# Kernel tuning notes

Measured on AMD Instinct MI355X. Metric: run time of the kernel, lower is better.

## Reference

```python
import jax, jax.numpy as jnp
import numpy as np

E = 512        # embedding_dim
DM = 512       # d_model
H = 8          # num_heads
HD = DM // H   # head_dim
NL = 4         # (e_num_layers-1) + (d_num_layers-1) identical VaeEncoder blocks
CIN = 32       # input_dim
EPS = 1e-5


def setup_inputs() -> dict:
    key = jax.random.key(0)
    ks = jax.random.split(key, 8)
    s = 0.02
    n = lambda k, shape: jax.random.normal(k, shape, jnp.float32) * s
    return {
        "x": jax.random.normal(ks[0], (4, 2048, CIN), jnp.float32),
        "conv_w": n(ks[1], (E, CIN, 3)),
        "conv_b": jnp.zeros((E,), jnp.float32),
        "qkv_w": n(ks[2], (NL, 3 * DM, E)),
        "qkv_b": jnp.zeros((NL, 3 * DM), jnp.float32),
        "out_w": n(ks[3], (NL, E, DM)),
        "out_b": jnp.zeros((NL, E), jnp.float32),
        "fc1_w": n(ks[4], (NL, E, E)),
        "fc1_b": jnp.zeros((NL, E), jnp.float32),
        "fc2_w": n(ks[5], (NL, E, E)),
        "fc2_b": jnp.zeros((NL, E), jnp.float32),
        "ln1_w": jnp.ones((NL, E), jnp.float32),
        "ln1_b": jnp.zeros((NL, E), jnp.float32),
        "ln2_w": jnp.ones((NL, E), jnp.float32),
        "ln2_b": jnp.zeros((NL, E), jnp.float32),
        "outp_w": n(ks[6], (CIN, E)),
        "outp_b": jnp.zeros((CIN,), jnp.float32),
    }


def _pos_embedding(L, d):
    pos = jnp.arange(L, dtype=jnp.float32)[:, None]
    div = jnp.exp(jnp.arange(0, d, 2, dtype=jnp.float32) * (-np.log(10000.0) / d))
    pe = jnp.zeros((L, d), jnp.float32)
    pe = pe.at[:, 0::2].set(jnp.sin(pos * div))
    pe = pe.at[:, 1::2].set(jnp.cos(pos * div))
    return pe


def _layernorm(x, w, b):
    mu = jnp.mean(x, axis=-1, keepdims=True)
    xc = x - mu
    inv = jax.lax.rsqrt(jnp.mean(xc * xc, axis=-1, keepdims=True) + EPS)
    return xc * inv * w + b


def _encoder_block(x, p):
    (qkv_w, qkv_b, out_w, out_b, fc1_w, fc1_b, fc2_w, fc2_b,
     ln1_w, ln1_b, ln2_w, ln2_b) = p
    B, L, _ = x.shape
    qkv = x @ qkv_w.T + qkv_b                      # [B, L, 3*DM]
    q = qkv[:, :, :DM].reshape(B, L, H, HD)
    k = qkv[:, :, DM:2 * DM].reshape(B, L, H, HD)
    v = qkv[:, :, 2 * DM:].reshape(B, L, H, HD)
    scores = jnp.einsum('bqhd,bkhd->bhqk', q, k)   # [B, H, L, L]
    attn = jax.nn.softmax(scores / jnp.sqrt(jnp.float32(HD)), axis=-1)
    ctx = jnp.einsum('bhqk,bkhd->bqhd', attn, v).reshape(B, L, DM)
    x = _layernorm(x + (ctx @ out_w.T + out_b), ln1_w, ln1_b)
    h = jax.nn.silu(x @ fc1_w.T + fc1_b) @ fc2_w.T + fc2_b
    return _layernorm(x + h, ln2_w, ln2_b)


def reference(x, conv_w, conv_b, qkv_w, qkv_b, out_w, out_b,
              fc1_w, fc1_b, fc2_w, fc2_b, ln1_w, ln1_b, ln2_w, ln2_b,
              outp_w, outp_b):
    B, L, _ = x.shape
    # TokenEmbedding: circular Conv1d k=3 pad=1 over the time axis
    xc = jnp.pad(x.transpose(0, 2, 1), ((0, 0), (0, 0), (1, 1)), mode='wrap')
    h = jax.lax.conv_general_dilated(
        xc, conv_w, (1,), 'VALID',
        dimension_numbers=('NCH', 'OIH', 'NCH')) + conv_b[None, :, None]
    h = h.transpose(0, 2, 1) + _pos_embedding(L, E)[None]
    params = (qkv_w, qkv_b, out_w, out_b, fc1_w, fc1_b, fc2_w, fc2_b,
              ln1_w, ln1_b, ln2_w, ln2_b)
    def step(carry, p):
        return _encoder_block(carry, p), None
    h, _ = jax.lax.scan(step, h, params)
    return h @ outp_w.T + outp_b
```

## Files before the change

kernel.cpp:

```cpp
#include <hip/hip_runtime.h>
#include <hip/hip_bf16.h>
#include <cstddef>

typedef short bf16x8 __attribute__((ext_vector_type(8)));
typedef float f32x4 __attribute__((ext_vector_type(4)));

__device__ __forceinline__ unsigned short f2bf(float x) {
  __hip_bfloat16 h = __float2bfloat16(x);
  unsigned short u; __builtin_memcpy(&u, &h, 2); return u;
}
__device__ __forceinline__ float bf2f(unsigned short u) {
  unsigned int v = ((unsigned int)u) << 16; float f; __builtin_memcpy(&f, &v, 4); return f;
}
__device__ __forceinline__ float swz16f(float x) {
  int i; __builtin_memcpy(&i, &x, 4);
  i = __builtin_amdgcn_ds_swizzle(i, 0x401F);
  float r; __builtin_memcpy(&r, &i, 4); return r;
}
__device__ __forceinline__ void gload16(const unsigned short* g, unsigned short* l) {
  __builtin_amdgcn_global_load_lds(
      (const __attribute__((address_space(1))) void*)g,
      (__attribute__((address_space(3))) void*)l, 16, 0, 0);
}
__device__ __forceinline__ void pipe_sync() {
  asm volatile("s_waitcnt vmcnt(0)" ::: "memory");
  __builtin_amdgcn_s_barrier();
  __builtin_amdgcn_sched_barrier(0);
}
__device__ __forceinline__ void bar_only() {
  asm volatile("" ::: "memory");
  __builtin_amdgcn_s_barrier();
  __builtin_amdgcn_sched_barrier(0);
}

__global__ __launch_bounds__(256) void cvt_all(
    const float* __restrict__ qkv_w, const float* __restrict__ out_w,
    const float* __restrict__ fc1_w, const float* __restrict__ fc2_w,
    const float* __restrict__ outp_w, unsigned short* __restrict__ dst)
{
  int i = blockIdx.x * 256 + threadIdx.x;
  if (i >= 1576960) return;
  const float* src; int off;
  if (i < 786432)       { src = qkv_w;  off = i; }
  else if (i < 1048576) { src = out_w;  off = i - 786432; }
  else if (i < 1310720) { src = fc1_w;  off = i - 1048576; }
  else if (i < 1572864) { src = fc2_w;  off = i - 1310720; }
  else                  { src = outp_w; off = i - 1572864; }
  float4 v = *(const float4*)(src + (size_t)off * 4);
  ushort4 o;
  o.x = f2bf(v.x); o.y = f2bf(v.y); o.z = f2bf(v.z); o.w = f2bf(v.w);
  *(ushort4*)(dst + (size_t)i * 4) = o;
}

__global__ __launch_bounds__(256) void conv_pe_kernel(
    const float* __restrict__ x, const float* __restrict__ cw,
    const float* __restrict__ cb, unsigned short* __restrict__ outb)
{
  const int L = 2048, CIN = 32;
  int b  = blockIdx.x >> 8;
  int l0 = (blockIdx.x & 255) << 3;
  int t  = threadIdx.x;
  __shared__ float xs[10][32];
  for (int idx = t; idx < 320; idx += 256) {
    int rr = idx >> 5, ci = idx & 31;
    int gl = (l0 - 1 + rr + L) & (L - 1);
    xs[rr][ci] = x[((size_t)b * L + gl) * CIN + ci];
  }
  __syncthreads();
  int e0 = t << 1;
  float acc0[8], acc1[8];
  float bb0 = cb[e0], bb1 = cb[e0 + 1];
#pragma unroll
  for (int li = 0; li < 8; li++) { acc0[li] = bb0; acc1[li] = bb1; }
  const float* w0p = cw + (size_t)e0 * 96;
  const float* w1p = w0p + 96;
  for (int ci = 0; ci < 32; ci++) {
#pragma unroll
    for (int kk = 0; kk < 3; kk++) {
      float w0 = w0p[ci * 3 + kk];
      float w1 = w1p[ci * 3 + kk];
#pragma unroll
      for (int li = 0; li < 8; li++) {
        float xv = xs[li + kk][ci];
        acc0[li] += xv * w0;
        acc1[li] += xv * w1;
      }
    }
  }
  float dv = __expf((float)e0 * (-9.210340371976184f / 512.0f));
#pragma unroll
  for (int li = 0; li < 8; li++) {
    int l = l0 + li;
    float arg = (float)l * dv;
    float sv = sinf(arg), cv = cosf(arg);
    size_t off = ((size_t)b * L + l) * 512 + e0;
    ushort2 ob; ob.x = f2bf(acc0[li] + sv); ob.y = f2bf(acc1[li] + cv);
    *(ushort2*)&outb[off] = ob;
  }
}

template<int EPI, int QSCALE, int NFR, int VOUT>
__global__ __launch_bounds__(256) void gemm_bf(
    const unsigned short* __restrict__ X,
    const unsigned short* __restrict__ W,
    const float* __restrict__ bias,
    const unsigned short* __restrict__ R,
    unsigned short* __restrict__ Yb,
    float* __restrict__ Yf,
    unsigned short* __restrict__ VT,
    int N)
{
  const int K = 512;
  constexpr int BN = NFR * 32;
  constexpr int WB = NFR * 4096;
  constexpr int BUF = 16384 + WB;
  __shared__ __align__(16) char smem[2 * BUF];
  int t = threadIdx.x;
  int lane = t & 63, wv = t >> 6;
  int g = lane >> 4, li = lane & 15;
  int m0 = (blockIdx.x & 63) << 7;
  int n0 = (blockIdx.x >> 6) * BN;
  int wm = (wv >> 1) << 6;
  int wn = (wv & 1) * (BN / 2);

  int subrow = lane >> 3;
  int coloff = ((lane & 7) ^ subrow) << 3;

  f32x4 acc[4][NFR];
#pragma unroll
  for (int a = 0; a < 4; a++)
#pragma unroll
    for (int b2 = 0; b2 < NFR; b2++) acc[a][b2] = (f32x4){0.f, 0.f, 0.f, 0.f};

#pragma unroll
  for (int j = 0; j < 4; j++) {
    int row = (wv * 4 + j) * 8 + subrow;
    gload16(X + (size_t)(m0 + row) * K + coloff,
            (unsigned short*)(smem + (wv * 4 + j) * 1024));
  }
#pragma unroll
  for (int j = 0; j < NFR; j++) {
    int row = (wv * NFR + j) * 8 + subrow;
    gload16(W + (size_t)(n0 + row) * K + coloff,
            (unsigned short*)(smem + 16384 + (wv * NFR + j) * 1024));
  }

#pragma unroll
  for (int ks = 0; ks < 8; ks++) {
    const int buf = ks & 1;
    char* cur = smem + buf * BUF;
    if (ks < 7) {
      char* nxt = smem + (buf ^ 1) * BUF;
      int k0 = (ks + 1) * 64;
#pragma unroll
      for (int j = 0; j < 4; j++) {
        int row = (wv * 4 + j) * 8 + subrow;
        gload16(X + (size_t)(m0 + row) * K + k0 + coloff,
                (unsigned short*)(nxt + (wv * 4 + j) * 1024));
      }
#pragma unroll
      for (int j = 0; j < NFR; j++) {
        int row = (wv * NFR + j) * 8 + subrow;
        gload16(W + (size_t)(n0 + row) * K + k0 + coloff,
                (unsigned short*)(nxt + 16384 + (wv * NFR + j) * 1024));
      }
      if constexpr (NFR == 4) asm volatile("s_waitcnt vmcnt(8)" ::: "memory");
      else if constexpr (NFR == 2) asm volatile("s_waitcnt vmcnt(6)" ::: "memory");
      else asm volatile("s_waitcnt vmcnt(5)" ::: "memory");
    } else {
      asm volatile("s_waitcnt vmcnt(0)" ::: "memory");
    }
    __builtin_amdgcn_s_barrier();
    __builtin_amdgcn_sched_barrier(0);

#pragma unroll
    for (int s = 0; s < 2; s++) {
      bf16x8 af[4], bfr[NFR];
#pragma unroll
      for (int mt = 0; mt < 4; mt++) {
        int row = wm + 16 * mt + li;
        af[mt] = *(const bf16x8*)(cur + (row * 8 + ((g + 4 * s) ^ (row & 7))) * 16);
      }
#pragma unroll
      for (int nt = 0; nt < NFR; nt++) {
        int row = wn + 16 * nt + li;
        bfr[nt] = *(const bf16x8*)(cur + 16384 +
                                   (row * 8 + ((g + 4 * s) ^ (row & 7))) * 16);
      }
#pragma unroll
      for (int mt = 0; mt < 4; mt++)
#pragma unroll
        for (int nt = 0; nt < NFR; nt++)
          acc[mt][nt] = __builtin_amdgcn_mfma_f32_16x16x32_bf16(
              af[mt], bfr[nt], acc[mt][nt], 0, 0, 0);
    }
    if (ks < 7) bar_only();
  }

  float bv[NFR];
#pragma unroll
  for (int nt = 0; nt < NFR; nt++) bv[nt] = bias[n0 + wn + 16 * nt + li];

  if (VOUT && n0 >= 1024) {
    unsigned short* Ts = (unsigned short*)smem;
    __builtin_amdgcn_s_barrier();
#pragma unroll
    for (int nt = 0; nt < NFR; nt++) {
      int col = wn + 16 * nt + li;
      float bvn = bv[nt];
#pragma unroll
      for (int mt = 0; mt < 4; mt++) {
        float v0 = acc[mt][nt][0] + bvn, v1 = acc[mt][nt][1] + bvn;
        float v2 = acc[mt][nt][2] + bvn, v3 = acc[mt][nt][3] + bvn;
        uint2 pk;
        asm("v_cvt_pk_bf16_f32 %0, %1, %2" : "=v"(pk.x) : "v"(v0), "v"(v1));
        asm("v_cvt_pk_bf16_f32 %0, %1, %2" : "=v"(pk.y) : "v"(v2), "v"(v3));
        *(uint2*)(Ts + col * 136 + wm + 16 * mt + 4 * g) = pk;
      }
    }
    __syncthreads();
    int vcol = t >> 1, half = t & 1;
    int gc = n0 - 1024 + vcol;
    int bh = (m0 >> 11) * 8 + (gc >> 6);
    int d  = gc & 63;
    unsigned short* dst = VT + ((size_t)bh * 64 + d) * 2048 + (m0 & 2047) + half * 64;
    const unsigned short* srcp = Ts + vcol * 136 + half * 64;
#pragma unroll
    for (int j2 = 0; j2 < 8; j2++)
      *(bf16x8*)(dst + j2 * 8) = *(const bf16x8*)(srcp + j2 * 8);
    return;
  }

#pragma unroll
  for (int mt = 0; mt < 4; mt++) {
#pragma unroll
    for (int i = 0; i < 4; i++) {
      size_t roff = (size_t)(m0 + wm + 16 * mt + 4 * g + i) * N;
#pragma unroll
      for (int nt = 0; nt < NFR; nt++) {
        int col = n0 + wn + 16 * nt + li;
        float v = acc[mt][nt][i] + bv[nt];
        if (EPI == 1) {
          v += bf2f(R[roff + col]);
          Yb[roff + col] = f2bf(v);
        } else if (EPI == 2) {
          v = v / (1.f + __expf(-v));
          Yb[roff + col] = f2bf(v);
        } else if (EPI == 3) {
          Yf[roff + col] = v;
        } else {
          if (QSCALE && col < 512) v *= 0.18033688011112042f;
          Yb[roff + col] = f2bf(v);
        }
      }
    }
  }
}

__global__ __launch_bounds__(256) void attn_mfma(
    const unsigned short* __restrict__ qkv,
    const unsigned short* __restrict__ Vt,
    unsigned short* __restrict__ ctx)
{
  const int L = 2048;
  int bh = blockIdx.x & 31, qi = blockIdx.x >> 5;
  int b = bh >> 3, h = bh & 7;
  int q0 = qi << 7;
  size_t tb = (size_t)b * L;
  int t = threadIdx.x, lane = t & 63, wv = t >> 6;
  int g = lane >> 4, li = lane & 15;
  int lisw = li & 7;

  __shared__ __align__(16) char smem[81920];

  int wq = q0 + wv * 32;
  bf16x8 qf00, qf01, qf10, qf11;
  {
    const unsigned short* qp0 = qkv + (tb + wq + li) * 1536 + h * 64 + g * 8;
    qf00 = *(const bf16x8*)qp0;
    qf01 = *(const bf16x8*)(qp0 + 32);
    const unsigned short* qp1 = qp0 + (size_t)16 * 1536;
    qf10 = *(const bf16x8*)qp1;
    qf11 = *(const bf16x8*)(qp1 + 32);
  }

  f32x4 accA[4], accB[4];
#pragma unroll
  for (int nt = 0; nt < 4; nt++) {
    accA[nt] = (f32x4){0.f, 0.f, 0.f, 0.f};
    accB[nt] = (f32x4){0.f, 0.f, 0.f, 0.f};
  }
  float lA = 0.f, lB = 0.f;

  int koff0 = li * 128 + ((g    ) ^ lisw) * 16;
  int koff1 = li * 128 + ((g + 4) ^ lisw) * 16;
  int vrowb = 16384 + li * 256;
  int vs00 = ((g    ) ^ lisw) << 4;
  int vs01 = ((g + 4) ^ lisw) << 4;
  int vs10 = ((8 + g) ^ lisw) << 4;
  int vs11 = ((12 + g) ^ lisw) << 4;
  const char* pb0 = smem + 65536 + wv * 4096 + li * 128 + ((g    ) ^ lisw) * 16;
  const char* pb1 = smem + 65536 + wv * 4096 + li * 128 + ((g + 4) ^ lisw) * 16;
  char* pwbase = smem + 65536 + wv * 4096 + li * 128 + ((g & 1) << 3);
  char* pw0 = pwbase + (((0 + (g >> 1)) ^ lisw) << 4);
  char* pw1 = pwbase + (((2 + (g >> 1)) ^ lisw) << 4);
  char* pw2 = pwbase + (((4 + (g >> 1)) ^ lisw) << 4);
  char* pw3 = pwbase + (((6 + (g >> 1)) ^ lisw) << 4);

  int subrow = lane >> 3;
  int coloff = ((lane & 7) ^ subrow) << 3;
  const unsigned short* kp[4];
  const unsigned short* vp[4];
#pragma unroll
  for (int j = 0; j < 4; j++) {
    int krow = (wv * 4 + j) * 8 + subrow;
    kp[j] = qkv + (tb + krow) * 1536 + 512 + h * 64 + coloff;
    int vrow = (wv * 4 + j) * 4 + g;
    vp[j] = Vt + ((size_t)bh * 64 + vrow) * 2048 + ((li ^ (vrow & 7)) << 3);
  }

#pragma unroll
  for (int j = 0; j < 4; j++) {
    gload16(kp[j], (unsigned short*)(smem + (wv * 4 + j) * 1024));
    gload16(vp[j], (unsigned short*)(smem + 16384 + (wv * 4 + j) * 1024));
    kp[j] += (size_t)128 * 1536; vp[j] += 128;
  }
  pipe_sync();

#pragma unroll 2
  for (int it = 0; it < 16; it++) {
    const int buf = it & 1;
    const char* base = smem + buf * 32768;
    if (it < 15) {
      char* nb = smem + (buf ^ 1) * 32768;
#pragma unroll
      for (int j = 0; j < 4; j++) {
        gload16(kp[j], (unsigned short*)(nb + (wv * 4 + j) * 1024));
        gload16(vp[j], (unsigned short*)(nb + 16384 + (wv * 4 + j) * 1024));
        kp[j] += (size_t)128 * 1536; vp[j] += 128;
      }
    }

    f32x4 sA[8], sB[8];
#pragma unroll
    for (int mt = 0; mt < 8; mt++) {
      sA[mt] = (f32x4){0.f, 0.f, 0.f, 0.f};
      sB[mt] = (f32x4){0.f, 0.f, 0.f, 0.f};
    }
    __builtin_amdgcn_s_setprio(1);
#pragma unroll
    for (int mt = 0; mt < 8; mt++) {
      bf16x8 kf = *(const bf16x8*)(base + koff0 + mt * 2048);
      sA[mt] = __builtin_amdgcn_mfma_f32_16x16x32_bf16(kf, qf00, sA[mt], 0, 0, 0);
      sB[mt] = __builtin_amdgcn_mfma_f32_16x16x32_bf16(kf, qf10, sB[mt], 0, 0, 0);
    }
#pragma unroll
    for (int mt = 0; mt < 8; mt++) {
      bf16x8 kf = *(const bf16x8*)(base + koff1 + mt * 2048);
      sA[mt] = __builtin_amdgcn_mfma_f32_16x16x32_bf16(kf, qf01, sA[mt], 0, 0, 0);
      sB[mt] = __builtin_amdgcn_mfma_f32_16x16x32_bf16(kf, qf11, sB[mt], 0, 0, 0);
    }
    __builtin_amdgcn_s_setprio(0);

    float psA = 0.f, psB = 0.f;
#define PBLK(SARR, PS, PWP, OFF)                                              \
    {                                                                         \
      float p0 = SARR[0], p1 = SARR[1], p2 = SARR[2], p3 = SARR[3];           \
      asm volatile("v_exp_f32 %0, %0\n\tv_exp_f32 %1, %1\n\t"                 \
                   "v_exp_f32 %2, %2\n\tv_exp_f32 %3, %3\n\ts_nop 1"          \
                   : "+v"(p0), "+v"(p1), "+v"(p2), "+v"(p3));                 \
      PS += (p0 + p1) + (p2 + p3);                                            \
      uint2 pv;                                                               \
      asm("v_cvt_pk_bf16_f32 %0, %1, %2" : "=v"(pv.x) : "v"(p0), "v"(p1));    \
      asm("v_cvt_pk_bf16_f32 %0, %1, %2" : "=v"(pv.y) : "v"(p2), "v"(p3));    \
      *(uint2*)(PWP + OFF) = pv;                                              \
    }
    PBLK(sA[0], psA, pw0, 0) PBLK(sA[1], psA, pw1, 0)
    PBLK(sA[2], psA, pw2, 0) PBLK(sA[3], psA, pw3, 0)
    PBLK(sB[0], psB, pw0, 2048) PBLK(sB[1], psB, pw1, 2048)
    PBLK(sB[2], psB, pw2, 2048) PBLK(sB[3], psB, pw3, 2048)
    {
      bf16x8 paA0 = *(const bf16x8*)(pb0);
      bf16x8 paB0 = *(const bf16x8*)(pb0 + 2048);
      __builtin_amdgcn_s_setprio(1);
#pragma unroll
      for (int nt = 0; nt < 4; nt++) {
        bf16x8 vb = *(const bf16x8*)(base + vrowb + nt * 4096 + vs00);
        accA[nt] = __builtin_amdgcn_mfma_f32_16x16x32_bf16(paA0, vb, accA[nt], 0, 0, 0);
        accB[nt] = __builtin_amdgcn_mfma_f32_16x16x32_bf16(paB0, vb, accB[nt], 0, 0, 0);
      }
      __builtin_amdgcn_s_setprio(0);
      bf16x8 paA1 = *(const bf16x8*)(pb1);
      bf16x8 paB1 = *(const bf16x8*)(pb1 + 2048);
      __builtin_amdgcn_s_setprio(1);
#pragma unroll
      for (int nt = 0; nt < 4; nt++) {
        bf16x8 vb = *(const bf16x8*)(base + vrowb + nt * 4096 + vs01);
        accA[nt] = __builtin_amdgcn_mfma_f32_16x16x32_bf16(paA1, vb, accA[nt], 0, 0, 0);
        accB[nt] = __builtin_amdgcn_mfma_f32_16x16x32_bf16(paB1, vb, accB[nt], 0, 0, 0);
      }
      __builtin_amdgcn_s_setprio(0);
    }
    PBLK(sA[4], psA, pw0, 0) PBLK(sA[5], psA, pw1, 0)
    PBLK(sA[6], psA, pw2, 0) PBLK(sA[7], psA, pw3, 0)
    PBLK(sB[4], psB, pw0, 2048) PBLK(sB[5], psB, pw1, 2048)
    PBLK(sB[6], psB, pw2, 2048) PBLK(sB[7], psB, pw3, 2048)
#undef PBLK
    {
      bf16x8 paA0 = *(const bf16x8*)(pb0);
      bf16x8 paB0 = *(const bf16x8*)(pb0 + 2048);
      __builtin_amdgcn_s_setprio(1);
#pragma unroll
      for (int nt = 0; nt < 4; nt++) {
        bf16x8 vb = *(const bf16x8*)(base + vrowb + nt * 4096 + vs10);
        accA[nt] = __builtin_amdgcn_mfma_f32_16x16x32_bf16(paA0, vb, accA[nt], 0, 0, 0);
        accB[nt] = __builtin_amdgcn_mfma_f32_16x16x32_bf16(paB0, vb, accB[nt], 0, 0, 0);
      }
      __builtin_amdgcn_s_setprio(0);
      bf16x8 paA1 = *(const bf16x8*)(pb1);
      bf16x8 paB1 = *(const bf16x8*)(pb1 + 2048);
      __builtin_amdgcn_s_setprio(1);
#pragma unroll
      for (int nt = 0; nt < 4; nt++) {
        bf16x8 vb = *(const bf16x8*)(base + vrowb + nt * 4096 + vs11);
        accA[nt] = __builtin_amdgcn_mfma_f32_16x16x32_bf16(paA1, vb, accA[nt], 0, 0, 0);
        accB[nt] = __builtin_amdgcn_mfma_f32_16x16x32_bf16(paB1, vb, accB[nt], 0, 0, 0);
      }
      __builtin_amdgcn_s_setprio(0);
    }
    psA += swz16f(psA); psA += __shfl_xor(psA, 32); lA += psA;
    psB += swz16f(psB); psB += __shfl_xor(psB, 32); lB += psB;

    pipe_sync();
  }

  float liA[4], liB[4];
#pragma unroll
  for (int i = 0; i < 4; i++) {
    liA[i] = 1.f / __shfl(lA, 4 * g + i);
    liB[i] = 1.f / __shfl(lB, 4 * g + i);
  }
#pragma unroll
  for (int i = 0; i < 4; i++) {
    size_t ra = (tb + wq + 4 * g + i) * 512 + h * 64;
    size_t rb = (tb + wq + 16 + 4 * g + i) * 512 + h * 64;
#pragma unroll
    for (int nt = 0; nt < 4; nt++) {
      ctx[ra + 16 * nt + li] = f2bf(accA[nt][i] * liA[i]);
      ctx[rb + 16 * nt + li] = f2bf(accB[nt][i] * liB[i]);
    }
  }
}

__global__ __launch_bounds__(256) void ln_kernel(
    const unsigned short* __restrict__ X, const float* __restrict__ g,
    const float* __restrict__ b, unsigned short* __restrict__ Yb)
{
  int t = threadIdx.x, lane = t & 63, wv = t >> 6;
  size_t row = (size_t)blockIdx.x * 4 + wv;
  bf16x8 xv = *(const bf16x8*)(X + row * 512 + lane * 8);
  float xf[8];
#pragma unroll
  for (int j = 0; j < 8; j++) xf[j] = bf2f((unsigned short)xv[j]);
  float sum = 0.f, sq = 0.f;
#pragma unroll
  for (int j = 0; j < 8; j++) { sum += xf[j]; sq += xf[j] * xf[j]; }
#pragma unroll
  for (int off = 32; off > 0; off >>= 1) {
    sum += __shfl_xor(sum, off);
    sq  += __shfl_xor(sq, off);
  }
  float mu  = sum * (1.0f / 512.0f);
  float inv = rsqrtf(sq * (1.0f / 512.0f) - mu * mu + 1e-5f);
  float4 g0 = *(const float4*)(g + lane * 8);
  float4 g1 = *(const float4*)(g + lane * 8 + 4);
  float4 b0 = *(const float4*)(b + lane * 8);
  float4 b1 = *(const float4*)(b + lane * 8 + 4);
  float gw[8] = {g0.x, g0.y, g0.z, g0.w, g1.x, g1.y, g1.z, g1.w};
  float bw[8] = {b0.x, b0.y, b0.z, b0.w, b1.x, b1.y, b1.z, b1.w};
  bf16x8 yb;
#pragma unroll
  for (int j = 0; j < 8; j++)
    yb[j] = (short)f2bf((xf[j] - mu) * inv * gw[j] + bw[j]);
  *(bf16x8*)(Yb + row * 512 + lane * 8) = yb;
}

extern "C" void kernel_launch(void* const* d_in, const int* in_sizes, int n_in,
                              void* d_out, int out_size, void* d_ws, size_t ws_size,
                              hipStream_t stream) {
  (void)in_sizes; (void)n_in; (void)out_size; (void)ws_size;
  const float* x      = (const float*)d_in[0];
  const float* conv_w = (const float*)d_in[1];
  const float* conv_b = (const float*)d_in[2];
  const float* qkv_w  = (const float*)d_in[3];
  const float* qkv_b  = (const float*)d_in[4];
  const float* out_w  = (const float*)d_in[5];
  const float* out_b  = (const float*)d_in[6];
  const float* fc1_w  = (const float*)d_in[7];
  const float* fc1_b  = (const float*)d_in[8];
  const float* fc2_w  = (const float*)d_in[9];
  const float* fc2_b  = (const float*)d_in[10];
  const float* ln1_w  = (const float*)d_in[11];
  const float* ln1_b  = (const float*)d_in[12];
  const float* ln2_w  = (const float*)d_in[13];
  const float* ln2_b  = (const float*)d_in[14];
  const float* outp_w = (const float*)d_in[15];
  const float* outp_b = (const float*)d_in[16];
  float* out = (float*)d_out;

  char* p = (char*)d_ws;
  unsigned short* A    = (unsigned short*)p;            p += (size_t)8192 * 512 * 2;
  unsigned short* QKV  = (unsigned short*)p;            p += (size_t)8192 * 1536 * 2;
  unsigned short* VT   = (unsigned short*)p;            p += (size_t)32 * 64 * 2048 * 2;
  unsigned short* CTX  = (unsigned short*)p;            p += (size_t)8192 * 512 * 2;
  unsigned short* Wq   = (unsigned short*)p;            p += (size_t)4 * 1536 * 512 * 2;
  unsigned short* Wo   = (unsigned short*)p;            p += (size_t)4 * 512 * 512 * 2;
  unsigned short* W1   = (unsigned short*)p;            p += (size_t)4 * 512 * 512 * 2;
  unsigned short* W2   = (unsigned short*)p;            p += (size_t)4 * 512 * 512 * 2;
  unsigned short* Wp   = (unsigned short*)p;            p += (size_t)32 * 512 * 2;
  unsigned short* D = QKV;

  cvt_all<<<6160, 256, 0, stream>>>(qkv_w, out_w, fc1_w, fc2_w, outp_w, Wq);

  conv_pe_kernel<<<1024, 256, 0, stream>>>(x, conv_w, conv_b, A);

  for (int l = 0; l < 4; l++) {
    gemm_bf<0, 1, 4, 1><<<64 * 12, 256, 0, stream>>>(
        A, Wq + (size_t)l * 1536 * 512, qkv_b + l * 1536, nullptr,
        QKV, nullptr, VT, 1536);
    attn_mfma<<<512, 256, 0, stream>>>(QKV, VT, CTX);
    gemm_bf<1, 0, 2, 0><<<64 * 8, 256, 0, stream>>>(
        CTX, Wo + (size_t)l * 512 * 512, out_b + l * 512, A,
        D, nullptr, nullptr, 512);
    ln_kernel<<<2048, 256, 0, stream>>>(D, ln1_w + l * 512, ln1_b + l * 512, A);
    gemm_bf<2, 0, 2, 0><<<64 * 8, 256, 0, stream>>>(
        A, W1 + (size_t)l * 512 * 512, fc1_b + l * 512, nullptr,
        CTX, nullptr, nullptr, 512);
    gemm_bf<1, 0, 2, 0><<<64 * 8, 256, 0, stream>>>(
        CTX, W2 + (size_t)l * 512 * 512, fc2_b + l * 512, A,
        D, nullptr, nullptr, 512);
    ln_kernel<<<2048, 256, 0, stream>>>(D, ln2_w + l * 512, ln2_b + l * 512, A);
  }
  gemm_bf<3, 0, 1, 0><<<64, 256, 0, stream>>>(
      A, Wp, outp_b, nullptr, nullptr, out, nullptr, 32);
}
```

Before: 481.4 us.

## Keep softmax probabilities in registers by permuting K rows to match MFMA layout

The attention kernel no longer writes exp'd scores to an LDS scratch region and reads them back as the PV MFMA A-operand. Instead, key rows are assigned to even/odd MFMA tiles with a matching swizzle so each lane's QK accumulator outputs can be packed directly into bf16x8 operands for the PV MFMAs. This removes the LDS round trip for P and shrinks shared memory from 80KB to 64KB, which may allow more resident blocks. The cost is more live registers for sixteen score accumulators and eight packed operands, plus a more intricate K load swizzle that must stay consistent with the V row order.

```diff
diff --git a/kernel.cpp b/kernel.cpp
--- a/kernel.cpp
+++ b/kernel.cpp
@@ -269,9 +269,9 @@
   size_t tb = (size_t)b * L;
   int t = threadIdx.x, lane = t & 63, wv = t >> 6;
   int g = lane >> 4, li = lane & 15;
-  int lisw = li & 7;
-
-  __shared__ __align__(16) char smem[81920];
+  int lisw7 = li & 7;
+
+  __shared__ __align__(16) char smem[65536];
 
   int wq = q0 + wv * 32;
   bf16x8 qf00, qf01, qf10, qf11;
@@ -292,29 +292,27 @@
   }
   float lA = 0.f, lB = 0.f;
 
-  int koff0 = li * 128 + ((g    ) ^ lisw) * 16;
-  int koff1 = li * 128 + ((g + 4) ^ lisw) * 16;
+  int rowE = ((li >> 2) << 3) + (li & 3);
+  int swzE = (li >> 2) << 1;
+  int swzO = swzE + 1;
+  int kE0 = rowE * 128 + ((g ^ swzE) << 4);
+  int kE1 = rowE * 128 + (((g + 4) ^ swzE) << 4);
+  int kO0 = (rowE + 4) * 128 + ((g ^ swzO) << 4);
+  int kO1 = (rowE + 4) * 128 + (((g + 4) ^ swzO) << 4);
   int vrowb = 16384 + li * 256;
-  int vs00 = ((g    ) ^ lisw) << 4;
-  int vs01 = ((g + 4) ^ lisw) << 4;
-  int vs10 = ((8 + g) ^ lisw) << 4;
-  int vs11 = ((12 + g) ^ lisw) << 4;
-  const char* pb0 = smem + 65536 + wv * 4096 + li * 128 + ((g    ) ^ lisw) * 16;
-  const char* pb1 = smem + 65536 + wv * 4096 + li * 128 + ((g + 4) ^ lisw) * 16;
-  char* pwbase = smem + 65536 + wv * 4096 + li * 128 + ((g & 1) << 3);
-  char* pw0 = pwbase + (((0 + (g >> 1)) ^ lisw) << 4);
-  char* pw1 = pwbase + (((2 + (g >> 1)) ^ lisw) << 4);
-  char* pw2 = pwbase + (((4 + (g >> 1)) ^ lisw) << 4);
-  char* pw3 = pwbase + (((6 + (g >> 1)) ^ lisw) << 4);
+  int vsl0 = ((g     ) ^ lisw7) << 4;
+  int vsl1 = ((g +  4) ^ lisw7) << 4;
+  int vsl2 = ((g +  8) ^ lisw7) << 4;
+  int vsl3 = ((g + 12) ^ lisw7) << 4;
 
   int subrow = lane >> 3;
-  int coloff = ((lane & 7) ^ subrow) << 3;
   const unsigned short* kp[4];
   const unsigned short* vp[4];
 #pragma unroll
   for (int j = 0; j < 4; j++) {
     int krow = (wv * 4 + j) * 8 + subrow;
-    kp[j] = qkv + (tb + krow) * 1536 + 512 + h * 64 + coloff;
+    int swzk = (2 * j + (subrow >> 2)) & 7;
+    kp[j] = qkv + (tb + krow) * 1536 + 512 + h * 64 + (((lane & 7) ^ swzk) << 3);
     int vrow = (wv * 4 + j) * 4 + g;
     vp[j] = Vt + ((size_t)bh * 64 + vrow) * 2048 + ((li ^ (vrow & 7)) << 3);
   }
@@ -341,93 +339,76 @@
       }
     }
 
-    f32x4 sA[8], sB[8];
-#pragma unroll
-    for (int mt = 0; mt < 8; mt++) {
-      sA[mt] = (f32x4){0.f, 0.f, 0.f, 0.f};
-      sB[mt] = (f32x4){0.f, 0.f, 0.f, 0.f};
-    }
+    f32x4 sEA0, sEA1, sEA2, sEA3, sOA0, sOA1, sOA2, sOA3;
+    f32x4 sEB0, sEB1, sEB2, sEB3, sOB0, sOB1, sOB2, sOB3;
+    const f32x4 kZ = {0.f, 0.f, 0.f, 0.f};
     __builtin_amdgcn_s_setprio(1);
-#pragma unroll
-    for (int mt = 0; mt < 8; mt++) {
-      bf16x8 kf = *(const bf16x8*)(base + koff0 + mt * 2048);
-      sA[mt] = __builtin_amdgcn_mfma_f32_16x16x32_bf16(kf, qf00, sA[mt], 0, 0, 0);
-      sB[mt] = __builtin_amdgcn_mfma_f32_16x16x32_bf16(kf, qf10, sB[mt], 0, 0, 0);
-    }
-#pragma unroll
-    for (int mt = 0; mt < 8; mt++) {
-      bf16x8 kf = *(const bf16x8*)(base + koff1 + mt * 2048);
-      sA[mt] = __builtin_amdgcn_mfma_f32_16x16x32_bf16(kf, qf01, sA[mt], 0, 0, 0);
-      sB[mt] = __builtin_amdgcn_mfma_f32_16x16x32_bf16(kf, qf11, sB[mt], 0, 0, 0);
-    }
+#define QKC(C, SEA, SOA, SEB, SOB)                                            \
+    {                                                                         \
+      bf16x8 k0 = *(const bf16x8*)(base + (C) * 4096 + kE0);                  \
+      bf16x8 k1 = *(const bf16x8*)(base + (C) * 4096 + kE1);                  \
+      SEA = __builtin_amdgcn_mfma_f32_16x16x32_bf16(k0, qf00, kZ, 0, 0, 0);   \
+      SEB = __builtin_amdgcn_mfma_f32_16x16x32_bf16(k0, qf10, kZ, 0, 0, 0);   \
+      SEA = __builtin_amdgcn_mfma_f32_16x16x32_bf16(k1, qf01, SEA, 0, 0, 0);  \
+      SEB = __builtin_amdgcn_mfma_f32_16x16x32_bf16(k1, qf11, SEB, 0, 0, 0);  \
+      bf16x8 k2 = *(const bf16x8*)(base + (C) * 4096 + kO0);                  \
+      bf16x8 k3 = *(const bf16x8*)(base + (C) * 4096 + kO1);                  \
+      SOA = __builtin_amdgcn_mfma_f32_16x16x32_bf16(k2, qf00, kZ, 0, 0, 0);   \
+      SOB = __builtin_amdgcn_mfma_f32_16x16x32_bf16(k2, qf10, kZ, 0, 0, 0);   \
+      SOA = __builtin_amdgcn_mfma_f32_16x16x32_bf16(k3, qf01, SOA, 0, 0, 0);  \
+      SOB = __builtin_amdgcn_mfma_f32_16x16x32_bf16(k3, qf11, SOB, 0, 0, 0);  \
+    }
+    QKC(0, sEA0, sOA0, sEB0, sOB0)
+    QKC(1, sEA1, sOA1, sEB1, sOB1)
+    QKC(2, sEA2, sOA2, sEB2, sOB2)
+    QKC(3, sEA3, sOA3, sEB3, sOB3)
+#undef QKC
     __builtin_amdgcn_s_setprio(0);
 
     float psA = 0.f, psB = 0.f;
-#define PBLK(SARR, PS, PWP, OFF)                                              \
+    bf16x8 paA0, paA1, paA2, paA3, paB0, paB1, paB2, paB3;
+#define EPACK(SE, SO, PS, PA)                                                 \
     {                                                                         \
-      float p0 = SARR[0], p1 = SARR[1], p2 = SARR[2], p3 = SARR[3];           \
+      float e0 = SE[0], e1 = SE[1], e2 = SE[2], e3 = SE[3];                   \
+      float o0 = SO[0], o1 = SO[1], o2 = SO[2], o3 = SO[3];                   \
       asm volatile("v_exp_f32 %0, %0\n\tv_exp_f32 %1, %1\n\t"                 \
                    "v_exp_f32 %2, %2\n\tv_exp_f32 %3, %3\n\ts_nop 1"          \
-                   : "+v"(p0), "+v"(p1), "+v"(p2), "+v"(p3));                 \
-      PS += (p0 + p1) + (p2 + p3);                                            \
-      uint2 pv;                                                               \
-      asm("v_cvt_pk_bf16_f32 %0, %1, %2" : "=v"(pv.x) : "v"(p0), "v"(p1));    \
-      asm("v_cvt_pk_bf16_f32 %0, %1, %2" : "=v"(pv.y) : "v"(p2), "v"(p3));    \
-      *(uint2*)(PWP + OFF) = pv;                                              \
-    }
-    PBLK(sA[0], psA, pw0, 0) PBLK(sA[1], psA, pw1, 0)
-    PBLK(sA[2], psA, pw2, 0) PBLK(sA[3], psA, pw3, 0)
-    PBLK(sB[0], psB, pw0, 2048) PBLK(sB[1], psB, pw1, 2048)
-    PBLK(sB[2], psB, pw2, 2048) PBLK(sB[3], psB, pw3, 2048)
-    {
-      bf16x8 paA0 = *(const bf16x8*)(pb0);
-      bf16x8 paB0 = *(const bf16x8*)(pb0 + 2048);
-      __builtin_amdgcn_s_setprio(1);
-#pragma unroll
-      for (int nt = 0; nt < 4; nt++) {
-        bf16x8 vb = *(const bf16x8*)(base + vrowb + nt * 4096 + vs00);
-        accA[nt] = __builtin_amdgcn_mfma_f32_16x16x32_bf16(paA0, vb, accA[nt], 0, 0, 0);
-        accB[nt] = __builtin_amdgcn_mfma_f32_16x16x32_bf16(paB0, vb, accB[nt], 0, 0, 0);
-      }
-      __builtin_amdgcn_s_setprio(0);
-      bf16x8 paA1 = *(const bf16x8*)(pb1);
-      bf16x8 paB1 = *(const bf16x8*)(pb1 + 2048);
-      __builtin_amdgcn_s_setprio(1);
-#pragma unroll
-      for (int nt = 0; nt < 4; nt++) {
-        bf16x8 vb = *(const bf16x8*)(base + vrowb + nt * 4096 + vs01);
-        accA[nt] = __builtin_amdgcn_mfma_f32_16x16x32_bf16(paA1, vb, accA[nt], 0, 0, 0);
-        accB[nt] = __builtin_amdgcn_mfma_f32_16x16x32_bf16(paB1, vb, accB[nt], 0, 0, 0);
-      }
-      __builtin_amdgcn_s_setprio(0);
-    }
-    PBLK(sA[4], psA, pw0, 0) PBLK(sA[5], psA, pw1, 0)
-    PBLK(sA[6], psA, pw2, 0) PBLK(sA[7], psA, pw3, 0)
-    PBLK(sB[4], psB, pw0, 2048) PBLK(sB[5], psB, pw1, 2048)
-    PBLK(sB[6], psB, pw2, 2048) PBLK(sB[7], psB, pw3, 2048)
-#undef PBLK
-    {
-      bf16x8 paA0 = *(const bf16x8*)(pb0);
-      bf16x8 paB0 = *(const bf16x8*)(pb0 + 2048);
-      __builtin_amdgcn_s_setprio(1);
-#pragma unroll
-      for (int nt = 0; nt < 4; nt++) {
-        bf16x8 vb = *(const bf16x8*)(base + vrowb + nt * 4096 + vs10);
-        accA[nt] = __builtin_amdgcn_mfma_f32_16x16x32_bf16(paA0, vb, accA[nt], 0, 0, 0);
-        accB[nt] = __builtin_amdgcn_mfma_f32_16x16x32_bf16(paB0, vb, accB[nt], 0, 0, 0);
-      }
-      __builtin_amdgcn_s_setprio(0);
-      bf16x8 paA1 = *(const bf16x8*)(pb1);
-      bf16x8 paB1 = *(const bf16x8*)(pb1 + 2048);
-      __builtin_amdgcn_s_setprio(1);
-#pragma unroll
-      for (int nt = 0; nt < 4; nt++) {
-        bf16x8 vb = *(const bf16x8*)(base + vrowb + nt * 4096 + vs11);
-        accA[nt] = __builtin_amdgcn_mfma_f32_16x16x32_bf16(paA1, vb, accA[nt], 0, 0, 0);
-        accB[nt] = __builtin_amdgcn_mfma_f32_16x16x32_bf16(paB1, vb, accB[nt], 0, 0, 0);
-      }
-      __builtin_amdgcn_s_setprio(0);
-    }
+                   : "+v"(e0), "+v"(e1), "+v"(e2), "+v"(e3));                 \
+      asm volatile("v_exp_f32 %0, %0\n\tv_exp_f32 %1, %1\n\t"                 \
+                   "v_exp_f32 %2, %2\n\tv_exp_f32 %3, %3\n\ts_nop 1"          \
+                   : "+v"(o0), "+v"(o1), "+v"(o2), "+v"(o3));                 \
+      PS += ((e0 + e1) + (e2 + e3)) + ((o0 + o1) + (o2 + o3));                \
+      unsigned int d0, d1, d2, d3;                                            \
+      asm("v_cvt_pk_bf16_f32 %0, %1, %2" : "=v"(d0) : "v"(e0), "v"(e1));      \
+      asm("v_cvt_pk_bf16_f32 %0, %1, %2" : "=v"(d1) : "v"(e2), "v"(e3));      \
+      asm("v_cvt_pk_bf16_f32 %0, %1, %2" : "=v"(d2) : "v"(o0), "v"(o1));      \
+      asm("v_cvt_pk_bf16_f32 %0, %1, %2" : "=v"(d3) : "v"(o2), "v"(o3));      \
+      unsigned int tmp_[4] = {d0, d1, d2, d3};                                \
+      __builtin_memcpy(&PA, tmp_, 16);                                        \
+    }
+    EPACK(sEA0, sOA0, psA, paA0) EPACK(sEA1, sOA1, psA, paA1)
+    EPACK(sEA2, sOA2, psA, paA2) EPACK(sEA3, sOA3, psA, paA3)
+    EPACK(sEB0, sOB0, psB, paB0) EPACK(sEB1, sOB1, psB, paB1)
+    EPACK(sEB2, sOB2, psB, paB2) EPACK(sEB3, sOB3, psB, paB3)
+#undef EPACK
+
+    __builtin_amdgcn_s_setprio(1);
+#define PVC(PAA, PAB, VS)                                                     \
+    {                                                                         \
+      _Pragma("unroll")                                                       \
+      for (int nt = 0; nt < 4; nt++) {                                        \
+        bf16x8 vb = *(const bf16x8*)(base + vrowb + nt * 4096 + (VS));        \
+        accA[nt] = __builtin_amdgcn_mfma_f32_16x16x32_bf16(PAA, vb, accA[nt], 0, 0, 0); \
+        accB[nt] = __builtin_amdgcn_mfma_f32_16x16x32_bf16(PAB, vb, accB[nt], 0, 0, 0); \
+      }                                                                       \
+    }
+    PVC(paA0, paB0, vsl0)
+    PVC(paA1, paB1, vsl1)
+    PVC(paA2, paB2, vsl2)
+    PVC(paA3, paB3, vsl3)
+#undef PVC
+    __builtin_amdgcn_s_setprio(0);
+
     psA += swz16f(psA); psA += __shfl_xor(psA, 32); lA += psA;
     psB += swz16f(psB); psB += __shfl_xor(psB, 32); lB += psB;
 
```

Measured after the change: 525.1 us. +9.1%, slower.
